# Kernel tuning notes

Measured on AMD Instinct MI355X. Metric: run time of the kernel, lower is better.

The kernel has to match this reference:

```python
import jax, jax.numpy as jnp
import numpy as np

# FP8 E4M3 pulse encoder constants (from init_kwargs defaults)
E_BITS = 4
M_BITS = 3
N_INT = 10          # scan_integer_bits
N_DEC = 10          # scan_decimal_bits
TOTAL_STEPS = N_INT + N_DEC
BIAS = 2 ** (E_BITS - 1) - 1        # 7
START_EXP = N_INT + BIAS            # down-counter start value (17)
SUB_START = N_INT + 6               # subnormal window start (== N_INT + BIAS - 1)


def setup_inputs() -> dict:
    key = jax.random.key(0)
    x = jax.random.normal(key, (8, 2048, 1024), dtype=jnp.float32)
    return {"x": x}


def _encode(x):
    dt = x.dtype
    shp = x.shape
    xf = x.reshape(-1)                      # [n]
    s_out = (xf < 0).astype(dt)             # sign bit (inhibitory SignBitNode)
    abs_x = jnp.abs(xf)
    n = xf.shape[0]

    def step(carry, t):
        V, has_fired, d, e_reg, m_reg = carry
        # DynamicThresholdIFNode: soft-reset IF, threshold 2^(N_INT-1-t)
        thr = jnp.exp2((N_INT - 1 - t).astype(dt))
        s = (V >= thr).astype(dt)
        V = V - s * thr
        # first-spike detection: fs = s AND NOT(has_fired)
        fs = s * (1.0 - has_fired)
        active = (t < SUB_START).astype(dt)  # scalar gate for normal-range latching
        # TemporalExponentGenerator: down-counter, LSB-first bits
        counter = jnp.maximum(START_EXP - 1 - t, 0)
        exp_bits = ((counter >> jnp.arange(E_BITS)) & 1).astype(dt)   # [E]
        # latch exponent at first spike (VecAND + VecOR accumulate)
        e_reg = jnp.maximum(e_reg, exp_bits[None, :] * (fs * active)[:, None])
        # delay line: d[:, i] holds fs(t-1-i); sample mantissa bits with current s
        m_reg = jnp.maximum(m_reg, s[:, None] * d)
        valid_fs = fs * active
        d = jnp.concatenate([valid_fs[:, None], d[:, :-1]], axis=1)
        # accumulate has_fired only during normal window
        has_fired = jnp.maximum(has_fired, fs * active)
        # subnormal window: directly sample m_reg[t - SUB_START] when never fired
        onehot = (jnp.arange(M_BITS) == (t - SUB_START)).astype(dt)   # [M]
        m_reg = jnp.maximum(m_reg, onehot[None, :] * (s * (1.0 - has_fired))[:, None])
        return (V, has_fired, d, e_reg, m_reg), None

    init = (abs_x,
            jnp.zeros((n,), dt),
            jnp.zeros((n, M_BITS), dt),
            jnp.zeros((n, E_BITS), dt),
            jnp.zeros((n, M_BITS), dt))
    (_, _, _, e_reg, m_reg), _ = jax.lax.scan(step, init, jnp.arange(TOTAL_STEPS))

    e_out = e_reg[:, ::-1]                   # LSB-first -> MSB-first (flip)
    out = jnp.concatenate([s_out[:, None], e_out, m_reg], axis=-1)
    return out.reshape(shp + (1 + E_BITS + M_BITS,))


def reference(x):
    return _encode(x)
```

## Files before the change

kernel.cpp:

```cpp
#include <hip/hip_runtime.h>


__device__ __forceinline__ void encode_one(float x, float4& lo, float4& hi) {
    float sign = (x < 0.0f) ? 1.0f : 0.0f;
    unsigned ub = __float_as_uint(x) & 0x7fffffffu;
    float a = __uint_as_float(ub);
    int e_lead = (int)(ub >> 23) - 127;

    int ec, mant;
    if (__builtin_expect(e_lead >= 10, 0)) {
        float V = a;
        int has_fired = 0, d0 = 0, d1 = 0, d2 = 0;
        int e_reg = 0, m0 = 0, m1 = 0, m2 = 0;
        for (int t = 0; t < 20; ++t) {
            float thr = __builtin_exp2f((float)(9 - t));
            int s = (V >= thr) ? 1 : 0;
            if (s) V -= thr;
            int fs = s & (has_fired ^ 1);
            int active = (t < 16) ? 1 : 0;
            int counter = (16 - t) > 0 ? (16 - t) : 0;
            if (fs & active) e_reg |= (counter & 15);
            if (s) { m0 |= d0; m1 |= d1; m2 |= d2; }
            int vfs = fs & active;
            d2 = d1; d1 = d0; d0 = vfs;
            has_fired |= vfs;
            if (t >= 16 && t <= 18) {
                int bit = s & (has_fired ^ 1);
                if (t == 16) m0 |= bit; else if (t == 17) m1 |= bit; else m2 |= bit;
            }
        }
        ec = e_reg;
        mant = (m0 << 2) | (m1 << 1) | m2;
    } else {
        bool norm = (e_lead >= -6);
        bool sub  = (e_lead >= -10) & !norm;
        int ec_n   = (7 + e_lead) & 15;
        int mant_n = (int)(ub >> 20) & 7;
        int mant_s = ((int)(a * 512.0f)) & 7;
        ec   = norm ? ec_n : 0;
        mant = norm ? mant_n : (sub ? mant_s : 0);
    }

    lo.x = sign;
    lo.y = (float)((ec >> 3) & 1);
    lo.z = (float)((ec >> 2) & 1);
    lo.w = (float)((ec >> 1) & 1);
    hi.x = (float)(ec & 1);
    hi.y = (float)((mant >> 2) & 1);
    hi.z = (float)((mant >> 1) & 1);
    hi.w = (float)(mant & 1);
}

__global__ __launch_bounds__(256) void pulse_encode_kernel(
        const float* __restrict__ in, float4* __restrict__ out, int n) {
    int i = blockIdx.x * 256 + threadIdx.x;
    if (i >= n) return;
    float4 lo, hi;
    encode_one(in[i], lo, hi);
    out[2 * i]     = lo;
    out[2 * i + 1] = hi;
}

extern "C" void kernel_launch(void* const* d_in, const int* in_sizes, int n_in,
                              void* d_out, int out_size, void* d_ws, size_t ws_size,
                              hipStream_t stream) {
    const float* x = (const float*)d_in[0];
    float4* out = (float4*)d_out;
    int n = in_sizes[0];
    int blocks = (n + 255) / 256;
    pulse_encode_kernel<<<blocks, 256, 0, stream>>>(x, out, n);
}
```

Measured before the change: 597.1 us.

## Vectorize input loads and stage output through swizzled LDS for coalesced stores

Each thread now loads a float4 of inputs and encodes four elements. The 32-byte outputs are staged in shared memory with an XOR swizzle and then written back as fully coalesced 16-byte nontemporal stores. A tail kernel handles any remainder. The aim is better memory efficiency on a heavily write-bound kernel, at the cost of 32KB of LDS per block and a barrier, which could reduce occupancy.

Result: faster. 552.4 us (median of 2 runs) (-7.5%).

```diff
diff --git a/kernel.cpp b/kernel.cpp
--- a/kernel.cpp
+++ b/kernel.cpp
@@ -1,7 +1,9 @@
 #include <hip/hip_runtime.h>
 
 
-__device__ __forceinline__ void encode_one(float x, float4& lo, float4& hi) {
+typedef float f32x4 __attribute__((ext_vector_type(4)));
+
+__device__ __forceinline__ void encode_one(float x, f32x4& lo, f32x4& hi) {
     float sign = (x < 0.0f) ? 1.0f : 0.0f;
     unsigned ub = __float_as_uint(x) & 0x7fffffffu;
     float a = __uint_as_float(ub);
@@ -52,10 +54,47 @@
 }
 
 __global__ __launch_bounds__(256) void pulse_encode_kernel(
-        const float* __restrict__ in, float4* __restrict__ out, int n) {
+        const f32x4* __restrict__ in4, f32x4* __restrict__ out4) {
+    __shared__ f32x4 lds[2048];
+    const int t = threadIdx.x;
+    const int blk = blockIdx.x;
+
+    f32x4 v = __builtin_nontemporal_load(&in4[blk * 256 + t]);
+
+    f32x4 lo0, hi0, lo1, hi1, lo2, hi2, lo3, hi3;
+    encode_one(v.x, lo0, hi0);
+    encode_one(v.y, lo1, hi1);
+    encode_one(v.z, lo2, hi2);
+    encode_one(v.w, lo3, hi3);
+
+    const int base = t * 8;
+    const int sw = t & 7;
+    lds[(base + 0) ^ sw] = lo0;
+    lds[(base + 1) ^ sw] = hi0;
+    lds[(base + 2) ^ sw] = lo1;
+    lds[(base + 3) ^ sw] = hi1;
+    lds[(base + 4) ^ sw] = lo2;
+    lds[(base + 5) ^ sw] = hi2;
+    lds[(base + 6) ^ sw] = lo3;
+    lds[(base + 7) ^ sw] = hi3;
+
+    __syncthreads();
+
+    const int obase = blk * 2048;
+    const int rsw = (t >> 3) & 7;
+#pragma unroll
+    for (int k = 0; k < 8; ++k) {
+        int s = t + 256 * k;
+        f32x4 val = lds[s ^ rsw];
+        __builtin_nontemporal_store(val, &out4[obase + s]);
+    }
+}
+
+__global__ __launch_bounds__(256) void pulse_encode_tail(
+        const float* __restrict__ in, f32x4* __restrict__ out, int n) {
     int i = blockIdx.x * 256 + threadIdx.x;
     if (i >= n) return;
-    float4 lo, hi;
+    f32x4 lo, hi;
     encode_one(in[i], lo, hi);
     out[2 * i]     = lo;
     out[2 * i + 1] = hi;
@@ -65,8 +104,17 @@
                               void* d_out, int out_size, void* d_ws, size_t ws_size,
                               hipStream_t stream) {
     const float* x = (const float*)d_in[0];
-    float4* out = (float4*)d_out;
+    f32x4* out = (f32x4*)d_out;
     int n = in_sizes[0];
-    int blocks = (n + 255) / 256;
-    pulse_encode_kernel<<<blocks, 256, 0, stream>>>(x, out, n);
+    int nblocks = n / 1024;
+    if (nblocks > 0) {
+        pulse_encode_kernel<<<nblocks, 256, 0, stream>>>(
+            (const f32x4*)x, out);
+    }
+    int done = nblocks * 1024;
+    int rem = n - done;
+    if (rem > 0) {
+        int tb = (rem + 255) / 256;
+        pulse_encode_tail<<<tb, 256, 0, stream>>>(x + done, out + 2 * done, rem);
+    }
 }
```

## Process two elements per thread and stage output through swizzled LDS for coalesced stores

Applied to the files above, without the earlier changes.

Each thread now loads two input floats with a nontemporal vector load and encodes both. The four output float4s per thread are written to XOR-swizzled shared memory, then read back so each store instruction covers a contiguous block, using nontemporal stores. The aim is fully coalesced streaming writes and fewer cache-polluting accesses on this bandwidth-bound kernel. In exchange it adds a barrier, LDS traffic, and a separate tail kernel for leftover elements.

New measurement: 561.3 us. -6.0%, faster.

```diff
diff --git a/kernel.cpp b/kernel.cpp
--- a/kernel.cpp
+++ b/kernel.cpp
@@ -1,7 +1,10 @@
 #include <hip/hip_runtime.h>
 
 
-__device__ __forceinline__ void encode_one(float x, float4& lo, float4& hi) {
+typedef float  f32x4 __attribute__((ext_vector_type(4)));
+typedef float  f32x2 __attribute__((ext_vector_type(2)));
+
+__device__ __forceinline__ void encode_one(float x, f32x4& lo, f32x4& hi) {
     float sign = (x < 0.0f) ? 1.0f : 0.0f;
     unsigned ub = __float_as_uint(x) & 0x7fffffffu;
     float a = __uint_as_float(ub);
@@ -51,11 +54,47 @@
     hi.w = (float)(mant & 1);
 }
 
-__global__ __launch_bounds__(256) void pulse_encode_kernel(
-        const float* __restrict__ in, float4* __restrict__ out, int n) {
+__global__ __launch_bounds__(256, 8) void pulse_encode_kernel(
+        const f32x2* __restrict__ in2, f32x4* __restrict__ out4) {
+    __shared__ f32x4 lds[1024];
+    const int t = threadIdx.x;
+    const int tile = blockIdx.x;
+
+    f32x2 v = __builtin_nontemporal_load(&in2[tile * 256 + t]);
+
+    {
+        f32x4 lo, hi;
+        encode_one(v.x, lo, hi);
+        int s0 = 4 * t;
+        lds[s0 ^ ((s0 >> 3) & 7)] = lo;
+        int s1 = 4 * t + 1;
+        lds[s1 ^ ((s1 >> 3) & 7)] = hi;
+    }
+    {
+        f32x4 lo, hi;
+        encode_one(v.y, lo, hi);
+        int s2 = 4 * t + 2;
+        lds[s2 ^ ((s2 >> 3) & 7)] = lo;
+        int s3 = 4 * t + 3;
+        lds[s3 ^ ((s3 >> 3) & 7)] = hi;
+    }
+
+    __syncthreads();
+
+    const int obase = tile * 1024;
+#pragma unroll
+    for (int k = 0; k < 4; ++k) {
+        int s = t + 256 * k;
+        f32x4 val = lds[s ^ ((s >> 3) & 7)];
+        __builtin_nontemporal_store(val, &out4[obase + s]);
+    }
+}
+
+__global__ __launch_bounds__(256) void pulse_encode_tail(
+        const float* __restrict__ in, f32x4* __restrict__ out, int n) {
     int i = blockIdx.x * 256 + threadIdx.x;
     if (i >= n) return;
-    float4 lo, hi;
+    f32x4 lo, hi;
     encode_one(in[i], lo, hi);
     out[2 * i]     = lo;
     out[2 * i + 1] = hi;
@@ -65,8 +104,17 @@
                               void* d_out, int out_size, void* d_ws, size_t ws_size,
                               hipStream_t stream) {
     const float* x = (const float*)d_in[0];
-    float4* out = (float4*)d_out;
+    f32x4* out = (f32x4*)d_out;
     int n = in_sizes[0];
-    int blocks = (n + 255) / 256;
-    pulse_encode_kernel<<<blocks, 256, 0, stream>>>(x, out, n);
+    int ntiles = n / 512;
+    if (ntiles > 0) {
+        pulse_encode_kernel<<<ntiles, 256, 0, stream>>>(
+            (const f32x2*)x, out);
+    }
+    int done = ntiles * 512;
+    int rem = n - done;
+    if (rem > 0) {
+        int tb = (rem + 255) / 256;
+        pulse_encode_tail<<<tb, 256, 0, stream>>>(x + done, out + 2 * done, rem);
+    }
 }
```
